# Kernel optimization log

Measured on AMD Instinct MI355X. Metric: run time of the kernel, lower is better.

The kernel has to match this reference:

```python
import jax, jax.numpy as jnp
import numpy as np

LN_EPS = 1e-5
NEG_INF = -1e30


def setup_inputs() -> dict:
    key = jax.random.key(0)
    ks = jax.random.split(key, 8)
    B, S, D_MODEL, Q_IN = 1, 2048, 1024, 512
    HI, DI = 16, 64            # indexer heads / head_dim
    H, DQK, DV = 8, 64, 64     # MLA heads, qk_head_dim, v_head_dim
    return {
        "x": jax.random.normal(ks[0], (B, S, D_MODEL), jnp.float32),
        "q_input": jax.random.normal(ks[1], (B, S, Q_IN), jnp.float32),
        "q": jax.random.normal(ks[2], (B, S, H, DQK), jnp.float32),
        "k": jax.random.normal(ks[3], (B, S, H, DQK), jnp.float32),
        "v": jax.random.normal(ks[4], (B, S, H, DV), jnp.float32),
        "w_q": jax.random.normal(ks[5], (Q_IN, HI * DI), jnp.float32) * (Q_IN ** -0.5),
        "w_k": jax.random.normal(ks[6], (D_MODEL, DI), jnp.float32) * (D_MODEL ** -0.5),
        "ln_g": jnp.ones((DI,), jnp.float32),
        "ln_b": jnp.zeros((DI,), jnp.float32),
        "w_weights": jax.random.normal(ks[7], (D_MODEL, HI), jnp.float32) * (D_MODEL ** -0.5),
        "top_k": 128,
    }


def _indexer_topk(x, q_input, w_q, w_k, ln_g, ln_b, w_weights, top_k):
    """Lightning indexer: per-head relevance scores -> weighted sum -> causal top-k indices."""
    B, S, _ = x.shape
    HI = w_weights.shape[1]
    DI = w_k.shape[1]
    qi = (q_input @ w_q).reshape(B, S, HI, DI)          # bqhd
    ki = x @ w_k                                         # bkd
    mu = ki.mean(-1, keepdims=True)
    var = ((ki - mu) ** 2).mean(-1, keepdims=True)
    ki = (ki - mu) * jax.lax.rsqrt(var + LN_EPS) * ln_g + ln_b
    # per-head weights; scores*w summed over h == (sum_h w*q) . k  (fused, same math)
    w = (x @ w_weights) * (HI ** -0.5)                   # bqh
    q_eff = jnp.einsum("bqhd,bqh->bqd", qi, w) * (DI ** -0.5)
    scores = jnp.einsum("bqd,bkd->bqk", q_eff, ki)       # [B,S,S]
    pos = jnp.arange(S)
    causal = jnp.where(pos[None, :] <= pos[:, None], 0.0, NEG_INF).astype(scores.dtype)
    scores = scores + causal[None]
    return jax.lax.top_k(scores, top_k)[1]               # [B,S,K]


def reference(x, q_input, q, k, v, w_q, w_k, ln_g, ln_b, w_weights, top_k):
    B, S, H, DQK = q.shape
    DV = v.shape[-1]
    idx = _indexer_topk(x, q_input, w_q, w_k, ln_g, ln_b, w_weights, top_k)  # [B,S,K]

    qh = q.transpose(0, 2, 1, 3)   # [B,H,Sq,D]
    kh = k.transpose(0, 2, 1, 3)   # [B,H,Sk,D]
    vh = v.transpose(0, 2, 1, 3)

    def gather(kv, ix):            # kv [Sk,D], ix [Sq,K] -> [Sq,K,D]
        return kv[ix]

    gather_h = jax.vmap(gather, in_axes=(0, None))       # over heads, shared idx
    gather_bh = jax.vmap(gather_h, in_axes=(0, 0))       # over batch
    k_sel = gather_bh(kh, idx)     # [B,H,Sq,K,D]
    v_sel = gather_bh(vh, idx)     # [B,H,Sq,K,Dv]

    att = jnp.einsum("bhqd,bhqkd->bhqk", qh, k_sel) * (DQK ** -0.5)
    pos = jnp.arange(S)
    valid = idx[:, None, :, :] <= pos[None, None, :, None]   # causal validity of gathered idx
    att = jnp.where(valid, att, NEG_INF)
    p = jax.nn.softmax(att, axis=-1)
    out = jnp.einsum("bhqk,bhqkd->bhqd", p, v_sel)
    return out.transpose(0, 2, 1, 3)   # [B,S,H,Dv]
```

## Files before the change

### kernel.cpp

```cpp
#include <hip/hip_runtime.h>
#include <hip/hip_bf16.h>
#include <math.h>

#define S 2048
#define DM 1024
#define QIN 512
#define HI 16
#define DI 64
#define NH 8
#define TOPK 128
#define LN_EPS 1e-5f
#define KP 8

typedef float f32x4 __attribute__((ext_vector_type(4)));
typedef short s16x8 __attribute__((ext_vector_type(8)));

__device__ __forceinline__ float wave_sum(float v){
#pragma unroll
  for (int o = 32; o; o >>= 1) v += __shfl_xor(v, o);
  return v;
}
__device__ __forceinline__ float wave_max(float v){
#pragma unroll
  for (int o = 32; o; o >>= 1) v = fmaxf(v, __shfl_xor(v, o));
  return v;
}
__device__ __forceinline__ unsigned short f2bf(float x){
  unsigned u = __float_as_uint(x);
  unsigned r = u + 0x7FFFu + ((u >> 16) & 1u);
  return (unsigned short)(r >> 16);
}
__device__ __forceinline__ float bf2f(unsigned short s){
  return __uint_as_float(((unsigned)s) << 16);
}

__global__ __launch_bounds__(256) void k_prep(const float* __restrict__ qin,
                                              unsigned short* __restrict__ Ah,
                                              unsigned short* __restrict__ Al,
                                              const float* __restrict__ k,
                                              unsigned short* __restrict__ kh,
                                              const float* __restrict__ v,
                                              unsigned short* __restrict__ vh){
  const int SEG0 = S * QIN / 4;
  const int SEG1 = S * NH * 64 / 4;
  int id = blockIdx.x * 256 + threadIdx.x;
  if (id < SEG0){
    float4 f = ((const float4*)qin)[id];
    ushort4 h, lo;
    h.x = f2bf(f.x); lo.x = f2bf(f.x - bf2f(h.x));
    h.y = f2bf(f.y); lo.y = f2bf(f.y - bf2f(h.y));
    h.z = f2bf(f.z); lo.z = f2bf(f.z - bf2f(h.z));
    h.w = f2bf(f.w); lo.w = f2bf(f.w - bf2f(h.w));
    ((ushort4*)Ah)[id] = h;
    ((ushort4*)Al)[id] = lo;
  } else if (id < SEG0 + SEG1){
    int j = id - SEG0;
    float4 f = ((const float4*)k)[j];
    ushort4 o;
    o.x = f2bf(f.x); o.y = f2bf(f.y); o.z = f2bf(f.z); o.w = f2bf(f.w);
    ((ushort4*)kh)[j] = o;
  } else {
    int j = id - SEG0 - SEG1;
    float4 f = ((const float4*)v)[j];
    ushort4 o;
    o.x = f2bf(f.x); o.y = f2bf(f.y); o.z = f2bf(f.z); o.w = f2bf(f.w);
    ((ushort4*)vh)[j] = o;
  }
}

__global__ __launch_bounds__(256) void k_trsplit(const float* __restrict__ wq,
                                                 unsigned short* __restrict__ bh,
                                                 unsigned short* __restrict__ bl){
  const int k0 = blockIdx.x * 32;
  const int n0 = blockIdx.y * 32;
  const int t = threadIdx.x;
  __shared__ unsigned short lh[32][33];
  __shared__ unsigned short ll[32][33];
  const int c = t & 31, r8 = t >> 5;
#pragma unroll
  for (int i = 0; i < 4; ++i){
    int kk = r8 + i * 8;
    float wv = wq[(size_t)(k0 + kk) * 1024 + n0 + c];
    unsigned short h = f2bf(wv);
    lh[c][kk] = h;
    ll[c][kk] = f2bf(wv - bf2f(h));
  }
  __syncthreads();
  const int kk = t & 31, nl = t >> 5;
#pragma unroll
  for (int i = 0; i < 4; ++i){
    int nn = nl + i * 8;
    bh[(size_t)(n0 + nn) * QIN + k0 + kk] = lh[nn][kk];
    bl[(size_t)(n0 + nn) * QIN + k0 + kk] = ll[nn][kk];
  }
}

__global__ __launch_bounds__(256) void k_part(const float* __restrict__ x,
                                              const float* __restrict__ wk,
                                              const float* __restrict__ ww,
                                              float* __restrict__ part){
  const int kp = blockIdx.x;
  const int bm = blockIdx.y;
  const int t  = threadIdx.x;
  const int m0 = bm * 64;
  __shared__ float As[32][68];
  __shared__ float Bs[32][84];
  const int tm = (t & 15) * 4;
  const int tn = (t >> 4) * 5;
  float acc[4][5];
#pragma unroll
  for (int i = 0; i < 4; i++)
#pragma unroll
    for (int j = 0; j < 5; j++) acc[i][j] = 0.f;

  for (int kb = 0; kb < (DM / KP) / 32; ++kb){
    const int k0 = kp * (DM / KP) + kb * 32;
#pragma unroll
    for (int i = 0; i < 2; i++){
      int u = t + i * 256;
      int m = u >> 3, c4 = u & 7;
      float4 a = *(const float4*)&x[(size_t)(m0 + m) * DM + k0 + c4 * 4];
      As[c4*4+0][m] = a.x; As[c4*4+1][m] = a.y; As[c4*4+2][m] = a.z; As[c4*4+3][m] = a.w;
    }
#pragma unroll
    for (int i = 0; i < 10; i++){
      int u = t + i * 256;
      int kk = u / 80, nn = u % 80;
      float val = (nn < 64) ? wk[(size_t)(k0 + kk) * 64 + nn]
                            : ww[(size_t)(k0 + kk) * 16 + (nn - 64)];
      Bs[kk][nn] = val;
    }
    __syncthreads();
#pragma unroll
    for (int k = 0; k < 32; ++k){
      float4 a = *(const float4*)&As[k][tm];
      float av[4] = {a.x, a.y, a.z, a.w};
      float bb[5];
#pragma unroll
      for (int j = 0; j < 5; j++) bb[j] = Bs[k][tn + j];
#pragma unroll
      for (int i = 0; i < 4; i++)
#pragma unroll
        for (int j = 0; j < 5; j++) acc[i][j] = fmaf(av[i], bb[j], acc[i][j]);
    }
    __syncthreads();
  }
  float* dst = part + (size_t)kp * S * 80;
#pragma unroll
  for (int i = 0; i < 4; i++)
#pragma unroll
    for (int j = 0; j < 5; j++)
      dst[(size_t)(m0 + tm + i) * 80 + tn + j] = acc[i][j];
}

__global__ __launch_bounds__(256) void k_lnw(const float* __restrict__ part,
                                             const float* __restrict__ g,
                                             const float* __restrict__ b,
                                             float* __restrict__ ki,
                                             float* __restrict__ wgt){
  const int s = blockIdx.x * 4 + (threadIdx.x >> 6);
  const int l = threadIdx.x & 63;
  float kv = 0.f;
#pragma unroll
  for (int p = 0; p < KP; p++) kv += part[(size_t)p * S * 80 + (size_t)s * 80 + l];
  float wv = 0.f;
  if (l < 16){
#pragma unroll
    for (int p = 0; p < KP; p++) wv += part[(size_t)p * S * 80 + (size_t)s * 80 + 64 + l];
  }
  float mu = wave_sum(kv) * (1.f / 64.f);
  float d  = kv - mu;
  float var = wave_sum(d * d) * (1.f / 64.f);
  float o = d * (1.f / sqrtf(var + LN_EPS)) * g[l] + b[l];
  ki[(size_t)s * 64 + l] = o;
  if (l < 16) wgt[(size_t)s * 16 + l] = wv * 0.25f;
}

__global__ __launch_bounds__(256) void k_qi_mfma(const unsigned short* __restrict__ Ah,
                                                 const unsigned short* __restrict__ Al,
                                                 const unsigned short* __restrict__ Bh,
                                                 const unsigned short* __restrict__ Bl,
                                                 float* __restrict__ qi){
  const int bn = blockIdx.x;
  const int bm = blockIdx.y;
  const int w = threadIdx.x >> 6, l = threadIdx.x & 63;
  const int m0 = bm * 64 + (w >> 1) * 32;
  const int n0 = bn * 64 + (w & 1) * 32;
  const int r = l & 15, kg = l >> 4;

  f32x4 acc00 = {0,0,0,0}, acc01 = {0,0,0,0}, acc10 = {0,0,0,0}, acc11 = {0,0,0,0};

  const size_t aoff = (size_t)(m0 + r) * QIN + kg * 8;
  const size_t boff = (size_t)(n0 + r) * QIN + kg * 8;
#pragma unroll 4
  for (int k0 = 0; k0 < QIN; k0 += 32){
    s16x8 ah0 = *(const s16x8*)(Ah + aoff + k0);
    s16x8 ah1 = *(const s16x8*)(Ah + aoff + 16 * QIN + k0);
    s16x8 al0 = *(const s16x8*)(Al + aoff + k0);
    s16x8 al1 = *(const s16x8*)(Al + aoff + 16 * QIN + k0);
    s16x8 bh0 = *(const s16x8*)(Bh + boff + k0);
    s16x8 bh1 = *(const s16x8*)(Bh + boff + 16 * QIN + k0);
    s16x8 bl0 = *(const s16x8*)(Bl + boff + k0);
    s16x8 bl1 = *(const s16x8*)(Bl + boff + 16 * QIN + k0);
    acc00 = __builtin_amdgcn_mfma_f32_16x16x32_bf16(ah0, bh0, acc00, 0, 0, 0);
    acc00 = __builtin_amdgcn_mfma_f32_16x16x32_bf16(ah0, bl0, acc00, 0, 0, 0);
    acc00 = __builtin_amdgcn_mfma_f32_16x16x32_bf16(al0, bh0, acc00, 0, 0, 0);
    acc01 = __builtin_amdgcn_mfma_f32_16x16x32_bf16(ah0, bh1, acc01, 0, 0, 0);
    acc01 = __builtin_amdgcn_mfma_f32_16x16x32_bf16(ah0, bl1, acc01, 0, 0, 0);
    acc01 = __builtin_amdgcn_mfma_f32_16x16x32_bf16(al0, bh1, acc01, 0, 0, 0);
    acc10 = __builtin_amdgcn_mfma_f32_16x16x32_bf16(ah1, bh0, acc10, 0, 0, 0);
    acc10 = __builtin_amdgcn_mfma_f32_16x16x32_bf16(ah1, bl0, acc10, 0, 0, 0);
    acc10 = __builtin_amdgcn_mfma_f32_16x16x32_bf16(al1, bh0, acc10, 0, 0, 0);
    acc11 = __builtin_amdgcn_mfma_f32_16x16x32_bf16(ah1, bh1, acc11, 0, 0, 0);
    acc11 = __builtin_amdgcn_mfma_f32_16x16x32_bf16(ah1, bl1, acc11, 0, 0, 0);
    acc11 = __builtin_amdgcn_mfma_f32_16x16x32_bf16(al1, bh1, acc11, 0, 0, 0);
  }
#pragma unroll
  for (int j = 0; j < 4; ++j){
    qi[(size_t)(m0 +  0 + kg * 4 + j) * 1024 + n0 +  0 + r] = acc00[j];
    qi[(size_t)(m0 +  0 + kg * 4 + j) * 1024 + n0 + 16 + r] = acc01[j];
    qi[(size_t)(m0 + 16 + kg * 4 + j) * 1024 + n0 +  0 + r] = acc10[j];
    qi[(size_t)(m0 + 16 + kg * 4 + j) * 1024 + n0 + 16 + r] = acc11[j];
  }
}

__global__ __launch_bounds__(256) void k_qeff(const float* __restrict__ qi,
                                              const float* __restrict__ wgt,
                                              float* __restrict__ qe){
  const int id = blockIdx.x * 256 + threadIdx.x;
  const int s = id >> 6, d = id & 63;
  float acc = 0.f;
#pragma unroll
  for (int h = 0; h < 16; h++)
    acc = fmaf(wgt[(size_t)s * 16 + h], qi[(size_t)s * 1024 + h * 64 + d], acc);
  qe[(size_t)s * 64 + d] = acc * 0.125f;
}

__global__ __launch_bounds__(256) void k_scores(const float* __restrict__ qe,
                                                const float* __restrict__ ki,
                                                float* __restrict__ sc){
  const int bj = blockIdx.x, bi = blockIdx.y;
  if (bj > bi) return;
  const int t = threadIdx.x;
  const int i0 = bi * 64, j0 = bj * 64;
  __shared__ float Qs[64][68];
  __shared__ float Ks[64][68];
#pragma unroll
  for (int u0 = 0; u0 < 4; ++u0){
    int u = t + u0 * 256;
    int r = u >> 4, d4 = u & 15;
    float4 a = *(const float4*)&qe[(size_t)(i0 + r) * 64 + d4 * 4];
    Qs[d4*4+0][r] = a.x; Qs[d4*4+1][r] = a.y; Qs[d4*4+2][r] = a.z; Qs[d4*4+3][r] = a.w;
    float4 b = *(const float4*)&ki[(size_t)(j0 + r) * 64 + d4 * 4];
    Ks[d4*4+0][r] = b.x; Ks[d4*4+1][r] = b.y; Ks[d4*4+2][r] = b.z; Ks[d4*4+3][r] = b.w;
  }
  __syncthreads();
  const int tm = (t & 15) * 4, tn = (t >> 4) * 4;
  float acc[4][4] = {};
#pragma unroll
  for (int d = 0; d < 64; ++d){
    float4 a = *(const float4*)&Qs[d][tm];
    float4 b = *(const float4*)&Ks[d][tn];
    float av[4] = {a.x, a.y, a.z, a.w}, bb[4] = {b.x, b.y, b.z, b.w};
#pragma unroll
    for (int i = 0; i < 4; i++)
#pragma unroll
      for (int j = 0; j < 4; j++) acc[i][j] = fmaf(av[i], bb[j], acc[i][j]);
  }
#pragma unroll
  for (int i = 0; i < 4; i++)
#pragma unroll
    for (int j = 0; j < 4; j++)
      sc[(size_t)(i0 + tm + i) * S + j0 + tn + j] = acc[i][j];
}

__global__ __launch_bounds__(256) void k_topk(const float* __restrict__ sc,
                                              int* __restrict__ idx,
                                              int* __restrict__ cnt){
  const int i = blockIdx.x, t = threadIdx.x;
  const int w = t >> 6, l = t & 63;
  const int n = i + 1;
  int* outr = idx + (size_t)i * TOPK;
  if (n <= TOPK){
    for (int m = t; m < n; m += 256) outr[m] = m;
    if (t == 0) cnt[i] = n;
    return;
  }
  __shared__ unsigned int keys[S];
  __shared__ int tl[S];
  __shared__ int hist[256];
  __shared__ int wtot[4];
  __shared__ int s_b, s_above, s_gt, s_eq;
  hist[t] = 0;
  __syncthreads();
  for (int j = t; j < n; j += 256){
    unsigned int u = __float_as_uint(sc[(size_t)i * S + j]);
    unsigned int kk = (u & 0x80000000u) ? ~u : (u | 0x80000000u);
    keys[j] = kk;
    atomicAdd(&hist[kk >> 24], 1);
  }
  __syncthreads();
  unsigned int prefix = 0;
  int rem = TOPK;
  for (int p = 3; p >= 0; --p){
    const int sh = p * 8;
    const int h = hist[t];
    int vsc = h;
#pragma unroll
    for (int off = 1; off < 64; off <<= 1){
      int u = __shfl_down(vsc, off);
      if (l + off < 64) vsc += u;
    }
    if (l == 0) wtot[w] = vsc;
    __syncthreads();
    int later = 0;
#pragma unroll
    for (int ww = 1; ww < 4; ++ww) if (ww > w) later += wtot[ww];
    const int excl = vsc + later - h;
    if (excl < rem && excl + h >= rem){ s_b = t; s_above = excl; }
    __syncthreads();
    prefix |= ((unsigned int)s_b) << sh;
    rem -= s_above;
    if (p > 0){
      hist[t] = 0;
      __syncthreads();
      const unsigned int himask = 0xFFFFFFFFu << sh;
      const int shn = sh - 8;
      for (int j = t; j < n; j += 256){
        unsigned int kk = keys[j];
        if ((kk & himask) == prefix) atomicAdd(&hist[(kk >> shn) & 255], 1);
      }
      __syncthreads();
    }
  }
  if (t == 0){ s_gt = 0; s_eq = 0; }
  __syncthreads();
  for (int j = t; j < n; j += 256){
    unsigned int kk = keys[j];
    if (kk > prefix){ int p = atomicAdd(&s_gt, 1); outr[p] = j; }
    else if (kk == prefix){ int p = atomicAdd(&s_eq, 1); tl[p] = j; }
  }
  __syncthreads();
  const int base = s_gt;
  if (s_eq == rem){
    for (int m = t; m < rem; m += 256) outr[base + m] = tl[m];
  } else if (t == 0){
    int taken = 0;
    for (int j = 0; j < n && taken < rem; ++j)
      if (keys[j] == prefix) outr[base + taken++] = j;
  }
  if (t == 0) cnt[i] = TOPK;
}

__global__ __launch_bounds__(256) void k_attn(const float* __restrict__ q,
                                              const unsigned short* __restrict__ kh,
                                              const unsigned short* __restrict__ vh,
                                              const int* __restrict__ idx,
                                              const int* __restrict__ cnt,
                                              float* __restrict__ out){
  const int i = blockIdx.x;
  const int w = threadIdx.x >> 6, l = threadIdx.x & 63;
  const int n = cnt[i];
  const int* irow = idx + (size_t)i * TOPK;

  __shared__ int   sidx[4][TOPK];
  __shared__ float sp[4][2][TOPK];

  sidx[w][l]      = (l < n)      ? irow[l]      : 0;
  sidx[w][l + 64] = (l + 64 < n) ? irow[l + 64] : 0;

  const int h0 = 2 * w, h1 = h0 + 1;
  const int g = l >> 3, gl = l & 7;
  const float* qrow = q + (size_t)i * (NH * 64);
  float qa[8], qb[8];
  {
    float4 a0 = *(const float4*)&qrow[h0 * 64 + gl * 8];
    float4 a1 = *(const float4*)&qrow[h0 * 64 + gl * 8 + 4];
    float4 b0 = *(const float4*)&qrow[h1 * 64 + gl * 8];
    float4 b1 = *(const float4*)&qrow[h1 * 64 + gl * 8 + 4];
    qa[0]=a0.x*0.125f; qa[1]=a0.y*0.125f; qa[2]=a0.z*0.125f; qa[3]=a0.w*0.125f;
    qa[4]=a1.x*0.125f; qa[5]=a1.y*0.125f; qa[6]=a1.z*0.125f; qa[7]=a1.w*0.125f;
    qb[0]=b0.x*0.125f; qb[1]=b0.y*0.125f; qb[2]=b0.z*0.125f; qb[3]=b0.w*0.125f;
    qb[4]=b1.x*0.125f; qb[5]=b1.y*0.125f; qb[6]=b1.z*0.125f; qb[7]=b1.w*0.125f;
  }
  asm volatile("" ::: "memory");

#pragma unroll 4
  for (int pass = 0; pass < TOPK / 8; ++pass){
    const int j = pass * 8 + g;
    const size_t base = (size_t)sidx[w][j] * (NH * 64);
    uint4 u0 = *(const uint4*)(kh + base + h0 * 64 + gl * 8);
    uint4 u1 = *(const uint4*)(kh + base + h1 * 64 + gl * 8);
    float d0 = 0.f, d1 = 0.f;
    d0 = fmaf(__uint_as_float(u0.x << 16),         qa[0], d0);
    d0 = fmaf(__uint_as_float(u0.x & 0xFFFF0000u), qa[1], d0);
    d0 = fmaf(__uint_as_float(u0.y << 16),         qa[2], d0);
    d0 = fmaf(__uint_as_float(u0.y & 0xFFFF0000u), qa[3], d0);
    d0 = fmaf(__uint_as_float(u0.z << 16),         qa[4], d0);
    d0 = fmaf(__uint_as_float(u0.z & 0xFFFF0000u), qa[5], d0);
    d0 = fmaf(__uint_as_float(u0.w << 16),         qa[6], d0);
    d0 = fmaf(__uint_as_float(u0.w & 0xFFFF0000u), qa[7], d0);
    d1 = fmaf(__uint_as_float(u1.x << 16),         qb[0], d1);
    d1 = fmaf(__uint_as_float(u1.x & 0xFFFF0000u), qb[1], d1);
    d1 = fmaf(__uint_as_float(u1.y << 16),         qb[2], d1);
    d1 = fmaf(__uint_as_float(u1.y & 0xFFFF0000u), qb[3], d1);
    d1 = fmaf(__uint_as_float(u1.z << 16),         qb[4], d1);
    d1 = fmaf(__uint_as_float(u1.z & 0xFFFF0000u), qb[5], d1);
    d1 = fmaf(__uint_as_float(u1.w << 16),         qb[6], d1);
    d1 = fmaf(__uint_as_float(u1.w & 0xFFFF0000u), qb[7], d1);
#pragma unroll
    for (int o = 1; o < 8; o <<= 1){ d0 += __shfl_xor(d0, o); d1 += __shfl_xor(d1, o); }
    if (gl == 0){ sp[w][0][j] = d0; sp[w][1][j] = d1; }
  }
  asm volatile("" ::: "memory");

  const bool v0 = (l < n), v1 = (l + 64 < n);
  {
    float s0 = v0 ? sp[w][0][l] : -1e30f, s1 = v1 ? sp[w][0][l + 64] : -1e30f;
    float m = wave_max(fmaxf(s0, s1));
    float e0 = v0 ? __expf(s0 - m) : 0.f;
    float e1 = v1 ? __expf(s1 - m) : 0.f;
    float inv = 1.f / wave_sum(e0 + e1);
    sp[w][0][l] = e0 * inv;
    sp[w][0][l + 64] = e1 * inv;
  }
  {
    float s0 = v0 ? sp[w][1][l] : -1e30f, s1 = v1 ? sp[w][1][l + 64] : -1e30f;
    float m = wave_max(fmaxf(s0, s1));
    float e0 = v0 ? __expf(s0 - m) : 0.f;
    float e1 = v1 ? __expf(s1 - m) : 0.f;
    float inv = 1.f / wave_sum(e0 + e1);
    sp[w][1][l] = e0 * inv;
    sp[w][1][l + 64] = e1 * inv;
  }
  asm volatile("" ::: "memory");

  const int j2 = l >> 5;
  const int hp = (l >> 4) & 1;
  const int hh = h0 + hp;
  const int g4 = l & 15;
  float o4[4] = {0.f, 0.f, 0.f, 0.f};
#pragma unroll 4
  for (int pass = 0; pass < TOPK / 2; ++pass){
    const int j = pass * 2 + j2;
    const size_t base = (size_t)sidx[w][j] * (NH * 64);
    ushort4 uv = *(const ushort4*)(vh + base + hh * 64 + g4 * 4);
    float p = sp[w][hp][j];
    o4[0] = fmaf(p, bf2f(uv.x), o4[0]);
    o4[1] = fmaf(p, bf2f(uv.y), o4[1]);
    o4[2] = fmaf(p, bf2f(uv.z), o4[2]);
    o4[3] = fmaf(p, bf2f(uv.w), o4[3]);
  }
#pragma unroll
  for (int e = 0; e < 4; ++e) o4[e] += __shfl_xor(o4[e], 32);
  if (l < 32)
    *(float4*)&out[((size_t)i * NH + hh) * 64 + g4 * 4] = make_float4(o4[0], o4[1], o4[2], o4[3]);
}

extern "C" void kernel_launch(void* const* d_in, const int* in_sizes, int n_in,
                              void* d_out, int out_size, void* d_ws, size_t ws_size,
                              hipStream_t stream){
  const float* x   = (const float*)d_in[0];
  const float* qin = (const float*)d_in[1];
  const float* q   = (const float*)d_in[2];
  const float* k   = (const float*)d_in[3];
  const float* v   = (const float*)d_in[4];
  const float* wq  = (const float*)d_in[5];
  const float* wk  = (const float*)d_in[6];
  const float* lng = (const float*)d_in[7];
  const float* lnb = (const float*)d_in[8];
  const float* ww  = (const float*)d_in[9];
  float* out = (float*)d_out;

  float* ws   = (float*)d_ws;
  float* part = ws;
  float* ki   = ws + 1310720;
  float* wgt  = ws + 1441792;
  float* qi   = ws + 1474560;
  float* qe   = ws + 3571712;
  float* sc   = ws + 3702784;
  int*   idx  = (int*)(ws + 7897088);
  int*   cnt  = (int*)(ws + 8159232);
  unsigned short* kh = (unsigned short*)part;
  unsigned short* vh = kh + (size_t)S * NH * 64;
  unsigned short* Ah = (unsigned short*)sc;
  unsigned short* Al = Ah + (size_t)S * QIN;
  unsigned short* Bh = Al + (size_t)S * QIN;
  unsigned short* Bl = Bh + (size_t)1024 * QIN;

  hipLaunchKernelGGL(k_part,    dim3(KP, 32), dim3(256), 0, stream, x, wk, ww, part);
  hipLaunchKernelGGL(k_lnw,     dim3(512),    dim3(256), 0, stream, part, lng, lnb, ki, wgt);
  hipLaunchKernelGGL(k_prep,    dim3(3072),   dim3(256), 0, stream, qin, Ah, Al, k, kh, v, vh);
  hipLaunchKernelGGL(k_trsplit, dim3(16, 32), dim3(256), 0, stream, wq, Bh, Bl);
  hipLaunchKernelGGL(k_qi_mfma, dim3(16, 32), dim3(256), 0, stream, Ah, Al, Bh, Bl, qi);
  hipLaunchKernelGGL(k_qeff,    dim3(512),    dim3(256), 0, stream, qi, wgt, qe);
  hipLaunchKernelGGL(k_scores,  dim3(32, 32), dim3(256), 0, stream, qe, ki, sc);
  hipLaunchKernelGGL(k_topk,    dim3(2048),   dim3(256), 0, stream, sc, idx, cnt);
  hipLaunchKernelGGL(k_attn,    dim3(2048),   dim3(256), 0, stream, q, kh, vh, idx, cnt, out);
}
```

Baseline: 121.3 us.

## Merge prep kernels, compact radix top-k candidates, use fp16 packed math in attention

Folds the weight transpose/split kernel into the prep kernel as extra blocks, saving one launch. Rewrites top-k radix select so later passes scan only a compacted candidate list instead of the whole row. Stores K/V as fp16 and computes QK dot products with packed half2 FMAs. The half-precision accumulation lowers accuracy and could change which entries are near ties, and tie-breaking now falls back to a serial min-index selection.

```diff
diff --git a/kernel.cpp b/kernel.cpp
--- a/kernel.cpp
+++ b/kernel.cpp
@@ -1,5 +1,6 @@
 #include <hip/hip_runtime.h>
 #include <hip/hip_bf16.h>
+#include <hip/hip_fp16.h>
 #include <math.h>
 
 #define S 2048
@@ -33,6 +34,11 @@
 __device__ __forceinline__ float bf2f(unsigned short s){
   return __uint_as_float(((unsigned)s) << 16);
 }
+__device__ __forceinline__ unsigned short f2h(float x){
+  return __half_as_ushort(__float2half_rn(x));
+}
+union UH2 { unsigned int u; __half2 h; };
+__device__ __forceinline__ __half2 as_half2(unsigned int u){ UH2 x; x.u = u; return x.h; }
 
 __global__ __launch_bounds__(256) void k_prep(const float* __restrict__ qin,
                                               unsigned short* __restrict__ Ah,
@@ -40,42 +46,45 @@
                                               const float* __restrict__ k,
                                               unsigned short* __restrict__ kh,
                                               const float* __restrict__ v,
-                                              unsigned short* __restrict__ vh){
+                                              unsigned short* __restrict__ vh,
+                                              const float* __restrict__ wq,
+                                              unsigned short* __restrict__ Bh,
+                                              unsigned short* __restrict__ Bl){
+  __shared__ unsigned short lh[32][33];
+  __shared__ unsigned short ll[32][33];
   const int SEG0 = S * QIN / 4;
   const int SEG1 = S * NH * 64 / 4;
-  int id = blockIdx.x * 256 + threadIdx.x;
-  if (id < SEG0){
-    float4 f = ((const float4*)qin)[id];
-    ushort4 h, lo;
-    h.x = f2bf(f.x); lo.x = f2bf(f.x - bf2f(h.x));
-    h.y = f2bf(f.y); lo.y = f2bf(f.y - bf2f(h.y));
-    h.z = f2bf(f.z); lo.z = f2bf(f.z - bf2f(h.z));
-    h.w = f2bf(f.w); lo.w = f2bf(f.w - bf2f(h.w));
-    ((ushort4*)Ah)[id] = h;
-    ((ushort4*)Al)[id] = lo;
-  } else if (id < SEG0 + SEG1){
-    int j = id - SEG0;
-    float4 f = ((const float4*)k)[j];
-    ushort4 o;
-    o.x = f2bf(f.x); o.y = f2bf(f.y); o.z = f2bf(f.z); o.w = f2bf(f.w);
-    ((ushort4*)kh)[j] = o;
-  } else {
-    int j = id - SEG0 - SEG1;
-    float4 f = ((const float4*)v)[j];
-    ushort4 o;
-    o.x = f2bf(f.x); o.y = f2bf(f.y); o.z = f2bf(f.z); o.w = f2bf(f.w);
-    ((ushort4*)vh)[j] = o;
-  }
-}
-
-__global__ __launch_bounds__(256) void k_trsplit(const float* __restrict__ wq,
-                                                 unsigned short* __restrict__ bh,
-                                                 unsigned short* __restrict__ bl){
-  const int k0 = blockIdx.x * 32;
-  const int n0 = blockIdx.y * 32;
+  const int bid = blockIdx.x;
+  if (bid < 3072){
+    int id = bid * 256 + threadIdx.x;
+    if (id < SEG0){
+      float4 f = ((const float4*)qin)[id];
+      ushort4 h, lo;
+      h.x = f2bf(f.x); lo.x = f2bf(f.x - bf2f(h.x));
+      h.y = f2bf(f.y); lo.y = f2bf(f.y - bf2f(h.y));
+      h.z = f2bf(f.z); lo.z = f2bf(f.z - bf2f(h.z));
+      h.w = f2bf(f.w); lo.w = f2bf(f.w - bf2f(h.w));
+      ((ushort4*)Ah)[id] = h;
+      ((ushort4*)Al)[id] = lo;
+    } else if (id < SEG0 + SEG1){
+      int j = id - SEG0;
+      float4 f = ((const float4*)k)[j];
+      ushort4 o;
+      o.x = f2h(f.x); o.y = f2h(f.y); o.z = f2h(f.z); o.w = f2h(f.w);
+      ((ushort4*)kh)[j] = o;
+    } else {
+      int j = id - SEG0 - SEG1;
+      float4 f = ((const float4*)v)[j];
+      ushort4 o;
+      o.x = f2h(f.x); o.y = f2h(f.y); o.z = f2h(f.z); o.w = f2h(f.w);
+      ((ushort4*)vh)[j] = o;
+    }
+    return;
+  }
+  const int b2 = bid - 3072;
+  const int k0 = (b2 & 15) * 32;
+  const int n0 = (b2 >> 4) * 32;
   const int t = threadIdx.x;
-  __shared__ unsigned short lh[32][33];
-  __shared__ unsigned short ll[32][33];
   const int c = t & 31, r8 = t >> 5;
 #pragma unroll
   for (int i = 0; i < 4; ++i){
@@ -90,8 +99,8 @@
 #pragma unroll
   for (int i = 0; i < 4; ++i){
     int nn = nl + i * 8;
-    bh[(size_t)(n0 + nn) * QIN + k0 + kk] = lh[nn][kk];
-    bl[(size_t)(n0 + nn) * QIN + k0 + kk] = ll[nn][kk];
+    Bh[(size_t)(n0 + nn) * QIN + k0 + kk] = lh[nn][kk];
+    Bl[(size_t)(n0 + nn) * QIN + k0 + kk] = ll[nn][kk];
   }
 }
 
@@ -287,11 +296,13 @@
     return;
   }
   __shared__ unsigned int keys[S];
-  __shared__ int tl[S];
+  __shared__ int lA[S];
+  __shared__ int lB[S];
   __shared__ int hist[256];
   __shared__ int wtot[4];
-  __shared__ int s_b, s_above, s_gt, s_eq;
+  __shared__ int s_b, s_above, s_out, s_m;
   hist[t] = 0;
+  if (t == 0) s_out = 0;
   __syncthreads();
   for (int j = t; j < n; j += 256){
     unsigned int u = __float_as_uint(sc[(size_t)i * S + j]);
@@ -300,10 +311,8 @@
     atomicAdd(&hist[kk >> 24], 1);
   }
   __syncthreads();
-  unsigned int prefix = 0;
   int rem = TOPK;
-  for (int p = 3; p >= 0; --p){
-    const int sh = p * 8;
+  {
     const int h = hist[t];
     int vsc = h;
 #pragma unroll
@@ -319,35 +328,74 @@
     const int excl = vsc + later - h;
     if (excl < rem && excl + h >= rem){ s_b = t; s_above = excl; }
     __syncthreads();
-    prefix |= ((unsigned int)s_b) << sh;
-    rem -= s_above;
-    if (p > 0){
-      hist[t] = 0;
-      __syncthreads();
-      const unsigned int himask = 0xFFFFFFFFu << sh;
-      const int shn = sh - 8;
-      for (int j = t; j < n; j += 256){
-        unsigned int kk = keys[j];
-        if ((kk & himask) == prefix) atomicAdd(&hist[(kk >> shn) & 255], 1);
-      }
-      __syncthreads();
-    }
-  }
-  if (t == 0){ s_gt = 0; s_eq = 0; }
+  }
+  int b = s_b;
+  rem -= s_above;
+  if (t == 0) s_m = 0;
   __syncthreads();
   for (int j = t; j < n; j += 256){
-    unsigned int kk = keys[j];
-    if (kk > prefix){ int p = atomicAdd(&s_gt, 1); outr[p] = j; }
-    else if (kk == prefix){ int p = atomicAdd(&s_eq, 1); tl[p] = j; }
+    int by = keys[j] >> 24;
+    if (by > b){ int p = atomicAdd(&s_out, 1); outr[p] = j; }
+    else if (by == b){ int p = atomicAdd(&s_m, 1); lA[p] = j; }
   }
   __syncthreads();
-  const int base = s_gt;
-  if (s_eq == rem){
-    for (int m = t; m < rem; m += 256) outr[base + m] = tl[m];
-  } else if (t == 0){
-    int taken = 0;
-    for (int j = 0; j < n && taken < rem; ++j)
-      if (keys[j] == prefix) outr[base + taken++] = j;
+  int m = s_m;
+  int* Lsrc = lA; int* Ldst = lB;
+  bool done = false;
+  if (m == rem){
+    int base = TOPK - rem;
+    for (int u = t; u < m; u += 256) outr[base + u] = Lsrc[u];
+    done = true;
+  }
+  for (int p = 2; p >= 0 && !done; --p){
+    const int sh = p * 8;
+    __syncthreads();
+    hist[t] = 0;
+    __syncthreads();
+    for (int u = t; u < m; u += 256) atomicAdd(&hist[(keys[Lsrc[u]] >> sh) & 255], 1);
+    __syncthreads();
+    {
+      const int h = hist[t];
+      int vsc = h;
+#pragma unroll
+      for (int off = 1; off < 64; off <<= 1){
+        int u = __shfl_down(vsc, off);
+        if (l + off < 64) vsc += u;
+      }
+      if (l == 0) wtot[w] = vsc;
+      __syncthreads();
+      int later = 0;
+#pragma unroll
+      for (int ww = 1; ww < 4; ++ww) if (ww > w) later += wtot[ww];
+      const int excl = vsc + later - h;
+      if (excl < rem && excl + h >= rem){ s_b = t; s_above = excl; }
+      __syncthreads();
+    }
+    b = s_b;
+    rem -= s_above;
+    if (t == 0) s_m = 0;
+    __syncthreads();
+    for (int u = t; u < m; u += 256){
+      int j = Lsrc[u]; int by = (keys[j] >> sh) & 255;
+      if (by > b){ int p2 = atomicAdd(&s_out, 1); outr[p2] = j; }
+      else if (by == b){ int p2 = atomicAdd(&s_m, 1); Ldst[p2] = j; }
+    }
+    __syncthreads();
+    m = s_m;
+    { int* tmp = Lsrc; Lsrc = Ldst; Ldst = tmp; }
+    if (m == rem){
+      int base = TOPK - rem;
+      for (int u = t; u < m; u += 256) outr[base + u] = Lsrc[u];
+      done = true;
+    }
+  }
+  if (!done && t == 0){
+    int base = TOPK - rem;
+    for (int a = 0; a < rem; ++a){
+      int mn = 1 << 30, pos = -1;
+      for (int u = 0; u < m; ++u){ int j = Lsrc[u]; if (j < mn){ mn = j; pos = u; } }
+      outr[base + a] = mn; Lsrc[pos] = 1 << 30;
+    }
   }
   if (t == 0) cnt[i] = TOPK;
 }
@@ -372,16 +420,20 @@
   const int h0 = 2 * w, h1 = h0 + 1;
   const int g = l >> 3, gl = l & 7;
   const float* qrow = q + (size_t)i * (NH * 64);
-  float qa[8], qb[8];
+  __half2 qa2[4], qb2[4];
   {
     float4 a0 = *(const float4*)&qrow[h0 * 64 + gl * 8];
     float4 a1 = *(const float4*)&qrow[h0 * 64 + gl * 8 + 4];
     float4 b0 = *(const float4*)&qrow[h1 * 64 + gl * 8];
     float4 b1 = *(const float4*)&qrow[h1 * 64 + gl * 8 + 4];
-    qa[0]=a0.x*0.125f; qa[1]=a0.y*0.125f; qa[2]=a0.z*0.125f; qa[3]=a0.w*0.125f;
-    qa[4]=a1.x*0.125f; qa[5]=a1.y*0.125f; qa[6]=a1.z*0.125f; qa[7]=a1.w*0.125f;
-    qb[0]=b0.x*0.125f; qb[1]=b0.y*0.125f; qb[2]=b0.z*0.125f; qb[3]=b0.w*0.125f;
-    qb[4]=b1.x*0.125f; qb[5]=b1.y*0.125f; qb[6]=b1.z*0.125f; qb[7]=b1.w*0.125f;
+    qa2[0] = __floats2half2_rn(a0.x * 0.125f, a0.y * 0.125f);
+    qa2[1] = __floats2half2_rn(a0.z * 0.125f, a0.w * 0.125f);
+    qa2[2] = __floats2half2_rn(a1.x * 0.125f, a1.y * 0.125f);
+    qa2[3] = __floats2half2_rn(a1.z * 0.125f, a1.w * 0.125f);
+    qb2[0] = __floats2half2_rn(b0.x * 0.125f, b0.y * 0.125f);
+    qb2[1] = __floats2half2_rn(b0.z * 0.125f, b0.w * 0.125f);
+    qb2[2] = __floats2half2_rn(b1.x * 0.125f, b1.y * 0.125f);
+    qb2[3] = __floats2half2_rn(b1.z * 0.125f, b1.w * 0.125f);
   }
   asm volatile("" ::: "memory");
 
@@ -391,23 +443,18 @@
     const size_t base = (size_t)sidx[w][j] * (NH * 64);
     uint4 u0 = *(const uint4*)(kh + base + h0 * 64 + gl * 8);
     uint4 u1 = *(const uint4*)(kh + base + h1 * 64 + gl * 8);
-    float d0 = 0.f, d1 = 0.f;
-    d0 = fmaf(__uint_as_float(u0.x << 16),         qa[0], d0);
-    d0 = fmaf(__uint_as_float(u0.x & 0xFFFF0000u), qa[1], d0);
-    d0 = fmaf(__uint_as_float(u0.y << 16),         qa[2], d0);
-    d0 = fmaf(__uint_as_float(u0.y & 0xFFFF0000u), qa[3], d0);
-    d0 = fmaf(__uint_as_float(u0.z << 16),         qa[4], d0);
-    d0 = fmaf(__uint_as_float(u0.z & 0xFFFF0000u), qa[5], d0);
-    d0 = fmaf(__uint_as_float(u0.w << 16),         qa[6], d0);
-    d0 = fmaf(__uint_as_float(u0.w & 0xFFFF0000u), qa[7], d0);
-    d1 = fmaf(__uint_as_float(u1.x << 16),         qb[0], d1);
-    d1 = fmaf(__uint_as_float(u1.x & 0xFFFF0000u), qb[1], d1);
-    d1 = fmaf(__uint_as_float(u1.y << 16),         qb[2], d1);
-    d1 = fmaf(__uint_as_float(u1.y & 0xFFFF0000u), qb[3], d1);
-    d1 = fmaf(__uint_as_float(u1.z << 16),         qb[4], d1);
-    d1 = fmaf(__uint_as_float(u1.z & 0xFFFF0000u), qb[5], d1);
-    d1 = fmaf(__uint_as_float(u1.w << 16),         qb[6], d1);
-    d1 = fmaf(__uint_as_float(u1.w & 0xFFFF0000u), qb[7], d1);
+    __half2 acc0 = __floats2half2_rn(0.f, 0.f);
+    __half2 acc1 = __floats2half2_rn(0.f, 0.f);
+    acc0 = __hfma2(as_half2(u0.x), qa2[0], acc0);
+    acc0 = __hfma2(as_half2(u0.y), qa2[1], acc0);
+    acc0 = __hfma2(as_half2(u0.z), qa2[2], acc0);
+    acc0 = __hfma2(as_half2(u0.w), qa2[3], acc0);
+    acc1 = __hfma2(as_half2(u1.x), qb2[0], acc1);
+    acc1 = __hfma2(as_half2(u1.y), qb2[1], acc1);
+    acc1 = __hfma2(as_half2(u1.z), qb2[2], acc1);
+    acc1 = __hfma2(as_half2(u1.w), qb2[3], acc1);
+    float d0 = __low2float(acc0) + __high2float(acc0);
+    float d1 = __low2float(acc1) + __high2float(acc1);
 #pragma unroll
     for (int o = 1; o < 8; o <<= 1){ d0 += __shfl_xor(d0, o); d1 += __shfl_xor(d1, o); }
     if (gl == 0){ sp[w][0][j] = d0; sp[w][1][j] = d1; }
@@ -444,12 +491,13 @@
   for (int pass = 0; pass < TOPK / 2; ++pass){
     const int j = pass * 2 + j2;
     const size_t base = (size_t)sidx[w][j] * (NH * 64);
-    ushort4 uv = *(const ushort4*)(vh + base + hh * 64 + g4 * 4);
+    uint2 uv = *(const uint2*)(vh + base + hh * 64 + g4 * 4);
+    __half2 v01 = as_half2(uv.x), v23 = as_half2(uv.y);
     float p = sp[w][hp][j];
-    o4[0] = fmaf(p, bf2f(uv.x), o4[0]);
-    o4[1] = fmaf(p, bf2f(uv.y), o4[1]);
-    o4[2] = fmaf(p, bf2f(uv.z), o4[2]);
-    o4[3] = fmaf(p, bf2f(uv.w), o4[3]);
+    o4[0] = fmaf(p, __low2float(v01),  o4[0]);
+    o4[1] = fmaf(p, __high2float(v01), o4[1]);
+    o4[2] = fmaf(p, __low2float(v23),  o4[2]);
+    o4[3] = fmaf(p, __high2float(v23), o4[3]);
   }
 #pragma unroll
   for (int e = 0; e < 4; ++e) o4[e] += __shfl_xor(o4[e], 32);
@@ -490,8 +538,7 @@
 
   hipLaunchKernelGGL(k_part,    dim3(KP, 32), dim3(256), 0, stream, x, wk, ww, part);
   hipLaunchKernelGGL(k_lnw,     dim3(512),    dim3(256), 0, stream, part, lng, lnb, ki, wgt);
-  hipLaunchKernelGGL(k_prep,    dim3(3072),   dim3(256), 0, stream, qin, Ah, Al, k, kh, v, vh);
-  hipLaunchKernelGGL(k_trsplit, dim3(16, 32), dim3(256), 0, stream, wq, Bh, Bl);
+  hipLaunchKernelGGL(k_prep,    dim3(3584),   dim3(256), 0, stream, qin, Ah, Al, k, kh, v, vh, wq, Bh, Bl);
   hipLaunchKernelGGL(k_qi_mfma, dim3(16, 32), dim3(256), 0, stream, Ah, Al, Bh, Bl, qi);
   hipLaunchKernelGGL(k_qeff,    dim3(512),    dim3(256), 0, stream, qi, wgt, qe);
   hipLaunchKernelGGL(k_scores,  dim3(32, 32), dim3(256), 0, stream, qe, ki, sc);
```

New measurement: 120.1 us. Within noise of the previous version (-1.0%).
